# Kernel tuning notes

Hardware: AMD Instinct MI355X
Metric: run time of the kernel (lower is better)

The kernel has to match this reference:

```python
import jax, jax.numpy as jnp
import numpy as np

SQRT_2_OVER_PI = float(np.sqrt(2.0 / np.pi))

def gelu(x):
    return 0.5 * x * (1.0 + jnp.tanh(SQRT_2_OVER_PI * (x + 0.044715 * x ** 3)))

def layer_norm(x, w, b, eps=1e-5):
    mean = jnp.mean(x, axis=-1, keepdims=True)
    var = jnp.var(x, axis=-1, keepdims=True)
    return (x - mean) / jnp.sqrt(var + eps) * w + b

B, S, D, H = 4, 2048, 768, 12
HD = D // H

def setup_inputs() -> dict:
    key = jax.random.key(0)
    ks = jax.random.split(key, 13)
    sc = lambda fan_in: 1.0 / np.sqrt(fan_in)
    return {
        "x": jax.random.normal(ks[0], (B, S, D), jnp.float32),
        "ln1_w": jnp.ones((D,), jnp.float32),
        "ln1_b": jnp.zeros((D,), jnp.float32),
        "w_attn": jax.random.normal(ks[1], (D, 3 * D), jnp.float32) * sc(D),
        "b_attn": jax.random.normal(ks[2], (3 * D,), jnp.float32) * 0.02,
        "w_proj": jax.random.normal(ks[3], (D, D), jnp.float32) * sc(D),
        "b_proj": jax.random.normal(ks[4], (D,), jnp.float32) * 0.02,
        "ln2_w": jnp.ones((D,), jnp.float32),
        "ln2_b": jnp.zeros((D,), jnp.float32),
        "w_fc": jax.random.normal(ks[5], (D, 4 * D), jnp.float32) * sc(D),
        "b_fc": jax.random.normal(ks[6], (4 * D,), jnp.float32) * 0.02,
        "w_fc_proj": jax.random.normal(ks[7], (4 * D, D), jnp.float32) * sc(4 * D),
        "b_fc_proj": jax.random.normal(ks[8], (D,), jnp.float32) * 0.02,
    }

def reference(x, ln1_w, ln1_b, w_attn, b_attn, w_proj, b_proj,
              ln2_w, ln2_b, w_fc, b_fc, w_fc_proj, b_fc_proj):
    batch, seq, dim = x.shape
    # --- causal self-attention on ln_1(x) ---
    h = layer_norm(x, ln1_w, ln1_b)
    qkv = h @ w_attn + b_attn                       # [B,S,3D]
    q, k, v = jnp.split(qkv, 3, axis=-1)
    qh = q.reshape(batch, seq, H, HD).transpose(0, 2, 1, 3)  # [B,H,S,hd]
    kh = k.reshape(batch, seq, H, HD).transpose(0, 2, 1, 3)
    vh = v.reshape(batch, seq, H, HD).transpose(0, 2, 1, 3)
    scores = jnp.einsum('bhqd,bhkd->bhqk', qh, kh) / np.sqrt(HD)  # [B,H,S,S]
    causal = jnp.tril(jnp.ones((seq, seq), bool))
    scores = jnp.where(causal, scores, -jnp.inf)
    probs = jax.nn.softmax(scores, axis=-1)
    attn = jnp.einsum('bhqk,bhkd->bhqd', probs, vh)  # [B,H,S,hd]
    attn = attn.transpose(0, 2, 1, 3).reshape(batch, seq, dim)
    x = x + attn @ w_proj + b_proj
    # --- MLP on ln_2(x) ---
    h = layer_norm(x, ln2_w, ln2_b)
    h = gelu(h @ w_fc + b_fc)
    x = x + h @ w_fc_proj + b_fc_proj
    return x
```

## Files before the change

### kernel.cpp

```cpp
#include <hip/hip_runtime.h>

typedef __bf16 bf16x8 __attribute__((ext_vector_type(8)));
typedef float f32x4 __attribute__((ext_vector_type(4)));
typedef unsigned short u16;
typedef u16 u16x8 __attribute__((ext_vector_type(8)));
typedef u16 u16x4 __attribute__((ext_vector_type(4)));

#define DEVI static __device__ __forceinline__

DEVI u16 f2bf(float f) {
  unsigned u = __float_as_uint(f);
  u += 0x7FFFu + ((u >> 16) & 1u);
  return (u16)(u >> 16);
}
DEVI float bf2f(u16 u) { return __uint_as_float(((unsigned)u) << 16); }

DEVI void gload_lds16(const void* g, void* l) {
  __builtin_amdgcn_global_load_lds((const __attribute__((address_space(1))) void*)g,
                                   (__attribute__((address_space(3))) void*)l, 16, 0, 0);
}

__global__ __launch_bounds__(256) void k_transpose_w(const float* __restrict__ in,
                                                     u16* __restrict__ out, int R, int C) {
  __shared__ float tile[64][65];
  const int t = threadIdx.x;
  const int c0 = blockIdx.x * 64, r0 = blockIdx.y * 64;
#pragma unroll
  for (int i = 0; i < 4; ++i) {
    int id = t + i * 256;
    int r = id >> 4, c4 = (id & 15) * 4;
    f32x4 v = *(const f32x4*)(in + (size_t)(r0 + r) * C + c0 + c4);
#pragma unroll
    for (int j = 0; j < 4; ++j) tile[r][c4 + j] = v[j];
  }
  __syncthreads();
  const int oc = t >> 2;
  const int rr = (t & 3) * 16;
  u16x8 lo, hi;
#pragma unroll
  for (int j = 0; j < 8; ++j) lo[j] = f2bf(tile[rr + j][oc]);
#pragma unroll
  for (int j = 0; j < 8; ++j) hi[j] = f2bf(tile[rr + 8 + j][oc]);
  u16* dst = out + (size_t)(c0 + oc) * R + r0 + rr;
  *(u16x8*)dst = lo;
  *(u16x8*)(dst + 8) = hi;
}

__global__ __launch_bounds__(256) void k_transpose_v(const u16* __restrict__ qkv,
                                                     u16* __restrict__ vt) {
  __shared__ u16 tile[64][72];
  const int t = threadIdx.x;
  const int bh = blockIdx.y;
  const int b = bh / 12, h = bh % 12;
  const int s0 = blockIdx.x * 64;
  const u16* src = qkv + (size_t)b * 2048 * 2304 + 1536 + h * 64;
#pragma unroll
  for (int i = 0; i < 2; ++i) {
    int id = t + i * 256;
    int r = id >> 3, c8 = (id & 7) * 8;
    *(u16x8*)&tile[r][c8] = *(const u16x8*)(src + (size_t)(s0 + r) * 2304 + c8);
  }
  __syncthreads();
  const int od = t >> 2;
  const int rr = (t & 3) * 16;
  u16x8 lo, hi;
#pragma unroll
  for (int j = 0; j < 8; ++j) lo[j] = tile[rr + j][od];
#pragma unroll
  for (int j = 0; j < 8; ++j) hi[j] = tile[rr + 8 + j][od];
  u16* dst = vt + ((size_t)bh * 64 + od) * 2048 + s0 + rr;
  *(u16x8*)dst = lo;
  *(u16x8*)(dst + 8) = hi;
}

__global__ __launch_bounds__(192) void k_layernorm(const float* __restrict__ x,
                                                   const float* __restrict__ w,
                                                   const float* __restrict__ bvec,
                                                   u16* __restrict__ out) {
  const int row = blockIdx.x, t = threadIdx.x;
  const float* xr = x + (size_t)row * 768;
  f32x4 v = *(const f32x4*)(xr + t * 4);
  float s = v[0] + v[1] + v[2] + v[3];
  float sq = v[0] * v[0] + v[1] * v[1] + v[2] * v[2] + v[3] * v[3];
#pragma unroll
  for (int m = 1; m < 64; m <<= 1) { s += __shfl_xor(s, m); sq += __shfl_xor(sq, m); }
  __shared__ float red[2][3];
  const int wv = t >> 6;
  if ((t & 63) == 0) { red[0][wv] = s; red[1][wv] = sq; }
  __syncthreads();
  s = red[0][0] + red[0][1] + red[0][2];
  sq = red[1][0] + red[1][1] + red[1][2];
  const float mean = s * (1.0f / 768.0f);
  const float var = sq * (1.0f / 768.0f) - mean * mean;
  const float rstd = rsqrtf(var + 1e-5f);
  f32x4 wv4 = *(const f32x4*)(w + t * 4);
  f32x4 bv4 = *(const f32x4*)(bvec + t * 4);
  u16x4 o;
#pragma unroll
  for (int j = 0; j < 4; ++j) o[j] = f2bf((v[j] - mean) * rstd * wv4[j] + bv4[j]);
  *(u16x4*)(out + (size_t)row * 768 + t * 4) = o;
}

#define EPI_QKV 0
#define EPI_RESID 1
#define EPI_GELU 2

template <int EPI>
__global__ __launch_bounds__(256) void k_gemm(const u16* __restrict__ A,
                                              const u16* __restrict__ BT,
                                              const float* __restrict__ bias,
                                              const float* __restrict__ resid,
                                              void* __restrict__ outp,
                                              int M, int N, int K) {
  __shared__ u16 As[128 * 32];
  __shared__ u16 Bs[128 * 32];
  const int t = threadIdx.x;
  const int lane = t & 63, w = t >> 6;
  const int l15 = lane & 15, l4 = lane >> 4;
  const int wr = w >> 1, wc = w & 1;
  const int m0 = blockIdx.y * 128, n0 = blockIdx.x * 128;

  f32x4 acc[4][4] = {};

  for (int kt = 0; kt < K; kt += 32) {
#pragma unroll
    for (int i = 0; i < 2; ++i) {
      int c = w * 128 + i * 64 + lane;
      int m = c >> 2, k16 = (c & 3) * 8;
      gload_lds16(A + (size_t)(m0 + m) * K + kt + k16, As + c * 8);
    }
#pragma unroll
    for (int i = 0; i < 2; ++i) {
      int c = w * 128 + i * 64 + lane;
      int n = c >> 2, k16 = (c & 3) * 8;
      gload_lds16(BT + (size_t)(n0 + n) * K + kt + k16, Bs + c * 8);
    }
    __syncthreads();
    bf16x8 af[4], bfr[4];
#pragma unroll
    for (int f = 0; f < 4; ++f)
      af[f] = *(const bf16x8*)(As + (wr * 64 + f * 16 + l15) * 32 + l4 * 8);
#pragma unroll
    for (int f = 0; f < 4; ++f)
      bfr[f] = *(const bf16x8*)(Bs + (wc * 64 + f * 16 + l15) * 32 + l4 * 8);
#pragma unroll
    for (int fi = 0; fi < 4; ++fi)
#pragma unroll
      for (int fj = 0; fj < 4; ++fj)
        acc[fi][fj] = __builtin_amdgcn_mfma_f32_16x16x32_bf16(af[fi], bfr[fj], acc[fi][fj], 0, 0, 0);
    __syncthreads();
  }

#pragma unroll
  for (int fi = 0; fi < 4; ++fi) {
    const int mbase = m0 + wr * 64 + fi * 16 + l4 * 4;
#pragma unroll
    for (int fj = 0; fj < 4; ++fj) {
      const int n = n0 + wc * 64 + fj * 16 + l15;
      const float bn = bias[n];
#pragma unroll
      for (int r = 0; r < 4; ++r) {
        const size_t idx = (size_t)(mbase + r) * N + n;
        float val = acc[fi][fj][r] + bn;
        if constexpr (EPI == EPI_QKV) {
          ((u16*)outp)[idx] = f2bf(val);
        } else if constexpr (EPI == EPI_RESID) {
          ((float*)outp)[idx] = val + resid[idx];
        } else {
          float g = 0.5f * val * (1.0f + tanhf(0.7978845608028654f * (val + 0.044715f * val * val * val)));
          ((u16*)outp)[idx] = f2bf(g);
        }
      }
    }
  }
}

__global__ __launch_bounds__(512) void k_attn(const u16* __restrict__ qkv,
                                              const u16* __restrict__ vt,
                                              u16* __restrict__ out) {
  __shared__ u16 Ks[64 * 72];
  __shared__ u16 Vs[64 * 72];
  __shared__ u16 Ps[8][16 * 72];
  const int t = threadIdx.x, lane = t & 63, w = t >> 6;
  const int l15 = lane & 15, l4 = lane >> 4;
  const int l44 = l4 * 4;
  const int qb = blockIdx.x, h = blockIdx.y, b = blockIdx.z;
  const int q0 = qb * 128;
  const int qw = q0 + w * 16;
  const u16* qbase = qkv + (size_t)b * 2048 * 2304 + h * 64;
  const u16* kbase = qbase + 768;
  const u16* vtb = vt + ((size_t)(b * 12 + h) * 64) * 2048;

  const int qrow = qw + l15;
  bf16x8 qf0, qf1;
  {
    const float PRE = 0.18033688011112042f;
    u16x8 r0 = *(const u16x8*)(qbase + (size_t)qrow * 2304 + l4 * 8);
    u16x8 r1 = *(const u16x8*)(qbase + (size_t)qrow * 2304 + 32 + l4 * 8);
    u16x8 s0, s1;
#pragma unroll
    for (int j = 0; j < 8; ++j) { s0[j] = f2bf(bf2f(r0[j]) * PRE); s1[j] = f2bf(bf2f(r1[j]) * PRE); }
    qf0 = *(bf16x8*)&s0;
    qf1 = *(bf16x8*)&s1;
  }

  float m_run = -1e30f, l_run = 0.f;
  f32x4 o_acc[4] = {};
  u16* pw = &Ps[w][0];
  const int qq = qw + l15;

  const int ntiles = 2 * qb + 2;
  const int sr = t >> 3, sc8 = (t & 7) * 8;

  for (int kt = 0; kt < ntiles; ++kt) {
    const int kv0 = kt * 64;
    *(u16x8*)&Ks[sr * 72 + sc8] = *(const u16x8*)(kbase + (size_t)(kv0 + sr) * 2304 + sc8);
    *(u16x8*)&Vs[sr * 72 + sc8] = *(const u16x8*)(vtb + (size_t)sr * 2048 + kv0 + sc8);
    __syncthreads();

    if (kv0 <= qw + 15) {
      f32x4 sa[4] = {};
#pragma unroll
      for (int c = 0; c < 4; ++c) {
        bf16x8 kf0 = *(const bf16x8*)(Ks + (c * 16 + l15) * 72 + l4 * 8);
        bf16x8 kf1 = *(const bf16x8*)(Ks + (c * 16 + l15) * 72 + 32 + l4 * 8);
        sa[c] = __builtin_amdgcn_mfma_f32_16x16x32_bf16(kf0, qf0, sa[c], 0, 0, 0);
        sa[c] = __builtin_amdgcn_mfma_f32_16x16x32_bf16(kf1, qf1, sa[c], 0, 0, 0);
      }

      if (kv0 + 63 > qw) {
#pragma unroll
        for (int c = 0; c < 4; ++c)
#pragma unroll
          for (int r = 0; r < 4; ++r)
            if (kv0 + c * 16 + l44 + r > qq) sa[c][r] = -1e30f;
      }

      float pm = fmaxf(fmaxf(sa[0][0], sa[0][1]), fmaxf(sa[0][2], sa[0][3]));
#pragma unroll
      for (int c = 1; c < 4; ++c)
        pm = fmaxf(pm, fmaxf(fmaxf(sa[c][0], sa[c][1]), fmaxf(sa[c][2], sa[c][3])));
      pm = fmaxf(pm, __shfl_xor(pm, 16));
      pm = fmaxf(pm, __shfl_xor(pm, 32));

      if (__any(pm > m_run + 8.0f)) {
        float mn = fmaxf(m_run, pm);
        float scq = exp2f(m_run - mn);
        m_run = mn;
        l_run *= scq;
#pragma unroll
        for (int r = 0; r < 4; ++r) {
          float s = __shfl(scq, l44 + r);
#pragma unroll
          for (int cd = 0; cd < 4; ++cd) o_acc[cd][r] *= s;
        }
      }

      float ls = 0.f;
      u16x4 pk[4];
#pragma unroll
      for (int c = 0; c < 4; ++c)
#pragma unroll
        for (int r = 0; r < 4; ++r) {
          float p = exp2f(sa[c][r] - m_run);
          ls += p;
          pk[c][r] = f2bf(p);
        }
      ls += __shfl_xor(ls, 16);
      ls += __shfl_xor(ls, 32);
      l_run += ls;

#pragma unroll
      for (int c = 0; c < 4; ++c)
        *(u16x4*)(pw + l15 * 72 + c * 16 + l44) = pk[c];

      bf16x8 pa0 = *(const bf16x8*)(pw + l15 * 72 + l4 * 8);
      bf16x8 pa1 = *(const bf16x8*)(pw + l15 * 72 + 32 + l4 * 8);

#pragma unroll
      for (int cd = 0; cd < 4; ++cd) {
        bf16x8 vf0 = *(const bf16x8*)(Vs + (cd * 16 + l15) * 72 + l4 * 8);
        bf16x8 vf1 = *(const bf16x8*)(Vs + (cd * 16 + l15) * 72 + 32 + l4 * 8);
        o_acc[cd] = __builtin_amdgcn_mfma_f32_16x16x32_bf16(pa0, vf0, o_acc[cd], 0, 0, 0);
        o_acc[cd] = __builtin_amdgcn_mfma_f32_16x16x32_bf16(pa1, vf1, o_acc[cd], 0, 0, 0);
      }
    }
    __syncthreads();
  }

  float lr[4];
#pragma unroll
  for (int r = 0; r < 4; ++r) lr[r] = 1.0f / __shfl(l_run, l44 + r);
#pragma unroll
  for (int cd = 0; cd < 4; ++cd)
#pragma unroll
    for (int r = 0; r < 4; ++r) {
      int qr = qw + l44 + r;
      out[((size_t)(b * 2048) + qr) * 768 + h * 64 + cd * 16 + l15] = f2bf(o_acc[cd][r] * lr[r]);
    }
}

extern "C" void kernel_launch(void* const* d_in, const int* in_sizes, int n_in,
                              void* d_out, int out_size, void* d_ws, size_t ws_size,
                              hipStream_t stream) {
  (void)in_sizes; (void)n_in; (void)out_size; (void)ws_size;
  const float* x      = (const float*)d_in[0];
  const float* ln1_w  = (const float*)d_in[1];
  const float* ln1_b  = (const float*)d_in[2];
  const float* w_attn = (const float*)d_in[3];
  const float* b_attn = (const float*)d_in[4];
  const float* w_proj = (const float*)d_in[5];
  const float* b_proj = (const float*)d_in[6];
  const float* ln2_w  = (const float*)d_in[7];
  const float* ln2_b  = (const float*)d_in[8];
  const float* w_fc   = (const float*)d_in[9];
  const float* b_fc   = (const float*)d_in[10];
  const float* w_fcp  = (const float*)d_in[11];
  const float* b_fcp  = (const float*)d_in[12];
  float* out = (float*)d_out;

  char* ws = (char*)d_ws;
  u16*   wt_attn = (u16*)(ws + 0);
  u16*   wt_proj = (u16*)(ws + 3538944);
  u16*   wt_fc   = (u16*)(ws + 4718592);
  u16*   wt_fcp  = (u16*)(ws + 9437184);
  u16*   h_ln    = (u16*)(ws + 14155776);
  u16*   qkv     = (u16*)(ws + 26738688);
  u16*   vtb     = (u16*)(ws + 64487424);
  u16*   h_gelu  = qkv;
  u16*   attn    = (u16*)(ws + 77070336);
  float* x2      = (float*)(ws + 89653248);

  k_transpose_w<<<dim3(36, 12), 256, 0, stream>>>(w_attn, wt_attn, 768, 2304);
  k_transpose_w<<<dim3(12, 12), 256, 0, stream>>>(w_proj, wt_proj, 768, 768);
  k_transpose_w<<<dim3(48, 12), 256, 0, stream>>>(w_fc, wt_fc, 768, 3072);
  k_transpose_w<<<dim3(12, 48), 256, 0, stream>>>(w_fcp, wt_fcp, 3072, 768);
  k_layernorm<<<8192, 192, 0, stream>>>(x, ln1_w, ln1_b, h_ln);
  k_gemm<EPI_QKV><<<dim3(18, 64), 256, 0, stream>>>(h_ln, wt_attn, b_attn, nullptr, qkv, 8192, 2304, 768);
  k_transpose_v<<<dim3(32, 48), 256, 0, stream>>>(qkv, vtb);
  k_attn<<<dim3(16, 12, 4), 512, 0, stream>>>(qkv, vtb, attn);
  k_gemm<EPI_RESID><<<dim3(6, 64), 256, 0, stream>>>(attn, wt_proj, b_proj, x, x2, 8192, 768, 768);
  k_layernorm<<<8192, 192, 0, stream>>>(x2, ln2_w, ln2_b, h_ln);
  k_gemm<EPI_GELU><<<dim3(24, 64), 256, 0, stream>>>(h_ln, wt_fc, b_fc, nullptr, h_gelu, 8192, 3072, 768);
  k_gemm<EPI_RESID><<<dim3(6, 64), 256, 0, stream>>>(h_gelu, wt_fcp, b_fcp, x2, out, 8192, 768, 3072);
}
```

Baseline: 475.1 us.

## Double-buffer attention K/V loads via direct-to-LDS, swizzle, reverse block order, cheaper GELU

The attention kernel now double-buffers K and V tiles using global_load_lds, so the next tile is prefetched while the current one is computed, and drops one barrier per iteration. LDS padding is replaced by an XOR swizzle to avoid bank conflicts. Query blocks are launched in reverse order so the longest causal blocks start first, and MFMA sections raise wave priority. The GELU epilogue replaces tanhf with an equivalent exp2-based sigmoid form to cut transcendental cost.

```diff
diff --git a/kernel.cpp b/kernel.cpp
--- a/kernel.cpp
+++ b/kernel.cpp
@@ -167,7 +167,8 @@
         } else if constexpr (EPI == EPI_RESID) {
           ((float*)outp)[idx] = val + resid[idx];
         } else {
-          float g = 0.5f * val * (1.0f + tanhf(0.7978845608028654f * (val + 0.044715f * val * val * val)));
+          float z2 = 1.5957691216057308f * (val + 0.044715f * val * val * val);
+          float g = val / (1.0f + exp2f(-1.4426950408889634f * z2));
           ((u16*)outp)[idx] = f2bf(g);
         }
       }
@@ -178,18 +179,27 @@
 __global__ __launch_bounds__(512) void k_attn(const u16* __restrict__ qkv,
                                               const u16* __restrict__ vt,
                                               u16* __restrict__ out) {
-  __shared__ u16 Ks[64 * 72];
-  __shared__ u16 Vs[64 * 72];
+  __shared__ u16 Ks[2][64 * 64];
+  __shared__ u16 Vs[2][64 * 64];
   __shared__ u16 Ps[8][16 * 72];
   const int t = threadIdx.x, lane = t & 63, w = t >> 6;
   const int l15 = lane & 15, l4 = lane >> 4;
   const int l44 = l4 * 4;
-  const int qb = blockIdx.x, h = blockIdx.y, b = blockIdx.z;
+  const int qb = (int)gridDim.x - 1 - (int)blockIdx.x;
+  const int h = blockIdx.y, b = blockIdx.z;
   const int q0 = qb * 128;
   const int qw = q0 + w * 16;
   const u16* qbase = qkv + (size_t)b * 2048 * 2304 + h * 64;
   const u16* kbase = qbase + 768;
   const u16* vtb = vt + ((size_t)(b * 12 + h) * 64) * 2048;
+
+  const int sr = t >> 3;
+  const int scx = (t & 7) ^ (sr & 7);
+  const size_t kgo = (size_t)sr * 2304 + scx * 8;
+  const size_t vgo = (size_t)sr * 2048 + scx * 8;
+
+  const int rx0 = ((l4 ^ (l15 & 7)) * 8);
+  const int rx1 = (((4 + l4) ^ (l15 & 7)) * 8);
 
   const int qrow = qw + l15;
   bf16x8 qf0, qf1;
@@ -210,23 +220,31 @@
   const int qq = qw + l15;
 
   const int ntiles = 2 * qb + 2;
-  const int sr = t >> 3, sc8 = (t & 7) * 8;
+
+  gload_lds16(kbase + kgo, (char*)&Ks[0][0] + t * 16);
+  gload_lds16(vtb + vgo, (char*)&Vs[0][0] + t * 16);
 
   for (int kt = 0; kt < ntiles; ++kt) {
+    __syncthreads();
+    if (kt + 1 < ntiles) {
+      const int nb = (kt + 1) & 1;
+      gload_lds16(kbase + (size_t)(kt + 1) * 64 * 2304 + kgo, (char*)&Ks[nb][0] + t * 16);
+      gload_lds16(vtb + (size_t)(kt + 1) * 64 + vgo, (char*)&Vs[nb][0] + t * 16);
+    }
     const int kv0 = kt * 64;
-    *(u16x8*)&Ks[sr * 72 + sc8] = *(const u16x8*)(kbase + (size_t)(kv0 + sr) * 2304 + sc8);
-    *(u16x8*)&Vs[sr * 72 + sc8] = *(const u16x8*)(vtb + (size_t)sr * 2048 + kv0 + sc8);
-    __syncthreads();
-
     if (kv0 <= qw + 15) {
+      const u16* kb = &Ks[kt & 1][0];
+      const u16* vb = &Vs[kt & 1][0];
       f32x4 sa[4] = {};
+      __builtin_amdgcn_s_setprio(1);
 #pragma unroll
       for (int c = 0; c < 4; ++c) {
-        bf16x8 kf0 = *(const bf16x8*)(Ks + (c * 16 + l15) * 72 + l4 * 8);
-        bf16x8 kf1 = *(const bf16x8*)(Ks + (c * 16 + l15) * 72 + 32 + l4 * 8);
+        bf16x8 kf0 = *(const bf16x8*)(kb + (c * 16 + l15) * 64 + rx0);
+        bf16x8 kf1 = *(const bf16x8*)(kb + (c * 16 + l15) * 64 + rx1);
         sa[c] = __builtin_amdgcn_mfma_f32_16x16x32_bf16(kf0, qf0, sa[c], 0, 0, 0);
         sa[c] = __builtin_amdgcn_mfma_f32_16x16x32_bf16(kf1, qf1, sa[c], 0, 0, 0);
       }
+      __builtin_amdgcn_s_setprio(0);
 
       if (kv0 + 63 > qw) {
 #pragma unroll
@@ -277,15 +295,16 @@
       bf16x8 pa0 = *(const bf16x8*)(pw + l15 * 72 + l4 * 8);
       bf16x8 pa1 = *(const bf16x8*)(pw + l15 * 72 + 32 + l4 * 8);
 
+      __builtin_amdgcn_s_setprio(1);
 #pragma unroll
       for (int cd = 0; cd < 4; ++cd) {
-        bf16x8 vf0 = *(const bf16x8*)(Vs + (cd * 16 + l15) * 72 + l4 * 8);
-        bf16x8 vf1 = *(const bf16x8*)(Vs + (cd * 16 + l15) * 72 + 32 + l4 * 8);
+        bf16x8 vf0 = *(const bf16x8*)(vb + (cd * 16 + l15) * 64 + rx0);
+        bf16x8 vf1 = *(const bf16x8*)(vb + (cd * 16 + l15) * 64 + rx1);
         o_acc[cd] = __builtin_amdgcn_mfma_f32_16x16x32_bf16(pa0, vf0, o_acc[cd], 0, 0, 0);
         o_acc[cd] = __builtin_amdgcn_mfma_f32_16x16x32_bf16(pa1, vf1, o_acc[cd], 0, 0, 0);
       }
-    }
-    __syncthreads();
+      __builtin_amdgcn_s_setprio(0);
+    }
   }
 
   float lr[4];
```

Measured after the change: 472.5 us. Within noise of the previous version (-0.6%).
